# Performance work log

Measured on AMD Instinct MI355X. Metric: run time of the kernel, lower is better.

The kernel has to match this reference:

```python
import jax, jax.numpy as jnp
import numpy as np

D_HEAD = 64
KERNEL = 7


def make_neighbourhood_mask(kernel: int, ch: int, cw: int) -> jnp.ndarray:
    """Boolean mask [ch*cw, ch*cw]; True where key is inside the query's k x k window."""
    h_ramp = jnp.arange(ch)
    w_ramp = jnp.arange(cw)
    h_pos, w_pos = jnp.meshgrid(h_ramp, w_ramp, indexing='ij')  # [ch, cw]
    start_h = jnp.clip(h_pos - kernel // 2, 0, ch - kernel)[..., None, None]
    end_h = start_h + kernel
    start_w = jnp.clip(w_pos - kernel // 2, 0, cw - kernel)[..., None, None]
    end_w = start_w + kernel
    h_range = h_ramp.reshape(1, 1, ch, 1)
    w_range = w_ramp.reshape(1, 1, 1, cw)
    mask = (h_range >= start_h) & (h_range < end_h) & (w_range >= start_w) & (w_range < end_w)
    return mask.reshape(ch * cw, ch * cw)


def setup_inputs() -> dict:
    key = jax.random.key(0)
    k1, k2, k3 = jax.random.split(key, 3)
    B, H, W, D = 2, 64, 64, 384
    x = jax.random.normal(k1, (B, H, W, D), dtype=jnp.float32)
    w_qkv = jax.random.normal(k2, (3 * D, D), dtype=jnp.float32) * 0.02
    w_out = jax.random.normal(k3, (D, D), dtype=jnp.float32) * 0.02
    return {"x": x, "w_qkv": w_qkv, "w_out": w_out}


def reference(x, w_qkv, w_out):
    B, H, W, D = x.shape
    nh = D // D_HEAD
    N = H * W
    # qkv projection: Linear(D, 3D, bias=False) -> x @ w_qkv.T
    qkv = jnp.einsum('bhwd,ed->bhwe', x, w_qkv)  # [B,H,W,3D]
    # 'n h w (t nh e) -> t n nh (h w) e'
    qkv = qkv.reshape(B, N, 3, nh, D_HEAD)
    qkv = jnp.transpose(qkv, (2, 0, 3, 1, 4))  # [3, B, nh, N, e]
    q, k, v = qkv[0], qkv[1], qkv[2]
    mask = make_neighbourhood_mask(KERNEL, H, W)  # [N, N] bool
    scale = 1.0 / jnp.sqrt(jnp.asarray(D_HEAD, dtype=x.dtype))
    scores = jnp.einsum('bnqe,bnke->bnqk', q, k) * scale  # [B,nh,N,N]
    neg = jnp.asarray(jnp.finfo(scores.dtype).min, dtype=scores.dtype)
    scores = jnp.where(mask[None, None], scores, neg)
    attn = jax.nn.softmax(scores, axis=-1)
    out = jnp.einsum('bnqk,bnke->bnqe', attn, v)  # [B,nh,N,e]
    # 'n nh (h w) e -> n h w (nh e)'
    out = jnp.transpose(out, (0, 2, 1, 3)).reshape(B, H, W, D)
    return jnp.einsum('bhwd,ed->bhwe', out, w_out)
```

## Files before the change

### kernel.cpp

```cpp
#include <hip/hip_runtime.h>
#include <hip/hip_bf16.h>

typedef __attribute__((ext_vector_type(8))) short bf16x8;
typedef __attribute__((ext_vector_type(4))) short s16x4;
typedef __attribute__((ext_vector_type(4))) float fx4;

#define MFMA16(a, b, c) __builtin_amdgcn_mfma_f32_16x16x32_bf16((a), (b), (c), 0, 0, 0)

__device__ __forceinline__ short f2bf(float f) {
  unsigned u = __float_as_uint(f);
  u += 0x7fffu + ((u >> 16) & 1u);
  return (short)(u >> 16);
}

__device__ __forceinline__ bf16x8 ldu16(const short* p) {
  bf16x8 v; __builtin_memcpy(&v, p, 16); return v;
}

__device__ __forceinline__ void gl_lds16(const short* g, short* l) {
  __builtin_amdgcn_global_load_lds((const __attribute__((address_space(1))) void*)(g),
                                   (__attribute__((address_space(3))) void*)(l), 16, 0, 0);
}

__global__ __launch_bounds__(256) void convert_k(
    const float* __restrict__ x, const float* __restrict__ wq, const float* __restrict__ wo,
    short* __restrict__ xb, short* __restrict__ wb, short* __restrict__ wob) {
  const int i4 = (blockIdx.x * 256 + threadIdx.x) * 4;
  {
    float4 v = *(const float4*)(x + i4);
    s16x4 s; s[0] = f2bf(v.x); s[1] = f2bf(v.y); s[2] = f2bf(v.z); s[3] = f2bf(v.w);
    *(s16x4*)(xb + i4) = s;
  }
  if (i4 < 1152 * 384) {
    float4 v = *(const float4*)(wq + i4);
    s16x4 s; s[0] = f2bf(v.x); s[1] = f2bf(v.y); s[2] = f2bf(v.z); s[3] = f2bf(v.w);
    *(s16x4*)(wb + i4) = s;
  }
  if (i4 < 384 * 384) {
    float4 v = *(const float4*)(wo + i4);
    s16x4 s; s[0] = f2bf(v.x); s[1] = f2bf(v.y); s[2] = f2bf(v.z); s[3] = f2bf(v.w);
    *(s16x4*)(wob + i4) = s;
  }
}

__global__ __launch_bounds__(256) void qkv_gemm(
    const short* __restrict__ A, const short* __restrict__ Bw,
    short* __restrict__ qb, short* __restrict__ kb, short* __restrict__ vb) {
  __shared__ __align__(16) short As[128 * 64];
  __shared__ __align__(16) short Bs[128 * 64];
  const int orig = (blockIdx.x & 7) * 72 + (blockIdx.x >> 3);
  const int mt = orig / 9, nt = orig % 9;
  const int m0 = mt * 128, n0 = nt * 128;
  const int tid = threadIdx.x;
  const int lane = tid & 63, w = tid >> 6;
  const int wr = w >> 1, wc = w & 1;
  const int l15 = lane & 15, l4 = lane >> 4;
  const int srow = lane >> 3;
  const int scol = ((lane & 7) ^ (srow & 7)) * 8;
  const fx4 vzero = {0.f, 0.f, 0.f, 0.f};
  fx4 acc[4][4];
#pragma unroll
  for (int i = 0; i < 4; i++)
#pragma unroll
    for (int j = 0; j < 4; j++) acc[i][j] = vzero;

  for (int kt = 0; kt < 384; kt += 64) {
    __syncthreads();
#pragma unroll
    for (int q = 0; q < 4; q++) {
      gl_lds16(A  + (size_t)(m0 + w * 32 + q * 8 + srow) * 384 + kt + scol, As + (w * 32 + q * 8) * 64);
      gl_lds16(Bw + (size_t)(n0 + w * 32 + q * 8 + srow) * 384 + kt + scol, Bs + (w * 32 + q * 8) * 64);
    }
    __syncthreads();
    bf16x8 af[4][2], bfr[4][2];
#pragma unroll
    for (int i = 0; i < 4; i++) {
      const int ra = wr * 64 + i * 16 + l15;
      const int rb = wc * 64 + i * 16 + l15;
#pragma unroll
      for (int kk = 0; kk < 2; kk++) {
        af[i][kk]  = *(const bf16x8*)(As + ra * 64 + (((kk * 4 + l4) ^ (ra & 7)) * 8));
        bfr[i][kk] = *(const bf16x8*)(Bs + rb * 64 + (((kk * 4 + l4) ^ (rb & 7)) * 8));
      }
    }
#pragma unroll
    for (int i = 0; i < 4; i++)
#pragma unroll
      for (int j = 0; j < 4; j++) {
        acc[i][j] = MFMA16(af[i][0], bfr[j][0], acc[i][j]);
        acc[i][j] = MFMA16(af[i][1], bfr[j][1], acc[i][j]);
      }
  }
#pragma unroll
  for (int j = 0; j < 4; j++) {
    const int e = n0 + wc * 64 + j * 16 + l15;
    const int t = e / 384;
    const int rem = e - t * 384;
    const int head = rem >> 6, d = rem & 63;
#pragma unroll
    for (int i = 0; i < 4; i++) {
      const int mb = m0 + wr * 64 + i * 16 + l4 * 4;
      const int b = mb >> 12, pix = mb & 4095;
      if (t == 2) {
        s16x4 s4;
#pragma unroll
        for (int r = 0; r < 4; r++) s4[r] = f2bf(acc[i][j][r]);
        *(s16x4*)(vb + ((size_t)(b * 6 + head) * 64 + d) * 4096 + pix) = s4;
      } else {
        short* __restrict__ dst = (t == 0) ? qb : kb;
#pragma unroll
        for (int r = 0; r < 4; r++)
          dst[((size_t)(b * 6 + head) * 4096 + pix + r) * 64 + d] = f2bf(acc[i][j][r]);
      }
    }
  }
}

__global__ __launch_bounds__(256) void natt_k(
    const short* __restrict__ qg, const short* __restrict__ kg, const short* __restrict__ vtg,
    short* __restrict__ ob) {
  __shared__ __align__(16) short lds[224 * 72];
  short* Ks = lds;
  short* Ps = lds;

  const int bid = (blockIdx.x & 7) * 96 + (blockIdx.x >> 3);
  const int tile = bid & 63, bh = bid >> 6;
  const int h0 = (tile >> 3) * 8, w0 = (tile & 7) * 8;
  const int ph0 = max(h0 - 3, 0);
  const int pw0 = min(max(w0 - 3, 0) & ~1, 48);
  const int prows = min(h0 + 4, 57) + 7 - ph0;
  const int pcols = min(w0 + 4, 57) + 7 - pw0;
  const short* kb  = kg  + (size_t)bh * 262144;
  const short* vtb = vtg + (size_t)bh * 262144;
  const short* qb  = qg  + (size_t)bh * 262144;
  const int tid = threadIdx.x;
  const int lane = tid & 63, w = tid >> 6;
  const int l15 = lane & 15, l4 = lane >> 4;

  const int nlo = min(max(h0 + 2 * w - 3, 0), 57) - ph0;

  for (int i = tid; i < 224 * 8; i += 256) {
    const int kk = i >> 3, dc = i & 7;
    const int kr = kk >> 4, kc = kk & 15;
    const int krc = min(kr, prows - 1), kcc = min(kc, pcols - 1);
    const int pix = (ph0 + krc) * 64 + (pw0 + kcc);
    *(bf16x8*)(Ks + kk * 72 + dc * 8) = *(const bf16x8*)(kb + pix * 64 + dc * 8);
  }
  __syncthreads();

  const int qa = w * 16 + l15;
  const int qpix = (h0 + (qa >> 3)) * 64 + (w0 + (qa & 7));
  const bf16x8 aq0 = *(const bf16x8*)(qb + qpix * 64 + l4 * 8);
  const bf16x8 aq1 = *(const bf16x8*)(qb + qpix * 64 + 32 + l4 * 8);

  const fx4 vzero = {0.f, 0.f, 0.f, 0.f};
  fx4 s[8];
#pragma unroll
  for (int nj = 0; nj < 8; nj++) s[nj] = vzero;
#pragma unroll
  for (int nj = 0; nj < 8; nj++) {
    const int n = nlo + nj;
    const bf16x8 b0 = *(const bf16x8*)(Ks + (n * 16 + l15) * 72 + l4 * 8);
    const bf16x8 b1 = *(const bf16x8*)(Ks + (n * 16 + l15) * 72 + 32 + l4 * 8);
    s[nj] = MFMA16(aq0, b0, s[nj]);
    s[nj] = MFMA16(aq1, b1, s[nj]);
  }

#pragma unroll
  for (int r = 0; r < 4; r++) {
    const int q = w * 16 + l4 * 4 + r;
    const int qh = h0 + (q >> 3), qw = w0 + (q & 7);
    const int sh = min(max(qh - 3, 0), 57) - ph0;
    const int sw = min(max(qw - 3, 0), 57) - pw0;
    float m = -1e30f;
#pragma unroll
    for (int nj = 0; nj < 8; nj++) {
      const int n = nlo + nj;
      const bool valid = (n >= sh) && (n < sh + 7) && (l15 >= sw) && (l15 < sw + 7);
      const float val = valid ? s[nj][r] * 0.125f : -1e30f;
      s[nj][r] = val;
      m = fmaxf(m, val);
    }
    m = fmaxf(m, __shfl_xor(m, 1));
    m = fmaxf(m, __shfl_xor(m, 2));
    m = fmaxf(m, __shfl_xor(m, 4));
    m = fmaxf(m, __shfl_xor(m, 8));
    float sum = 0.f;
#pragma unroll
    for (int nj = 0; nj < 8; nj++) {
      const float e = __expf(s[nj][r] - m);
      s[nj][r] = e;
      sum += e;
    }
    sum += __shfl_xor(sum, 1);
    sum += __shfl_xor(sum, 2);
    sum += __shfl_xor(sum, 4);
    sum += __shfl_xor(sum, 8);
    const float inv = 1.f / sum;
#pragma unroll
    for (int nj = 0; nj < 8; nj++) s[nj][r] *= inv;
  }

  __syncthreads();

#pragma unroll
  for (int nj = 0; nj < 8; nj++)
#pragma unroll
    for (int r = 0; r < 4; r++)
      Ps[(w * 16 + l4 * 4 + r) * 136 + nj * 16 + l15] = f2bf(s[nj][r]);

  __builtin_amdgcn_wave_barrier();

  fx4 o[4];
#pragma unroll
  for (int j = 0; j < 4; j++) o[j] = vzero;
#pragma unroll
  for (int ks = 0; ks < 4; ks++) {
    const bf16x8 pa = *(const bf16x8*)(Ps + (w * 16 + l15) * 136 + ks * 32 + l4 * 8);
    const int n = nlo + 2 * ks + (l4 >> 1);
    const int vp = (ph0 + min(n, prows - 1)) * 64 + pw0 + (l4 & 1) * 8;
#pragma unroll
    for (int j = 0; j < 4; j++) {
      const bf16x8 vf = ldu16(vtb + (size_t)(j * 16 + l15) * 4096 + vp);
      o[j] = MFMA16(pa, vf, o[j]);
    }
  }

  const int b = bh / 6, head = bh % 6;
#pragma unroll
  for (int j = 0; j < 4; j++) {
    const int d = j * 16 + l15;
#pragma unroll
    for (int r = 0; r < 4; r++) {
      const int q = w * 16 + l4 * 4 + r;
      const int pix = (h0 + (q >> 3)) * 64 + (w0 + (q & 7));
      ob[(size_t)(b * 4096 + pix) * 384 + head * 64 + d] = f2bf(o[j][r]);
    }
  }
}

__global__ __launch_bounds__(256) void out_gemm(
    const short* __restrict__ A, const short* __restrict__ Bw, float* __restrict__ out) {
  __shared__ __align__(16) short As[64 * 64];
  __shared__ __align__(16) short Bs[64 * 64];
  const int orig = (blockIdx.x & 7) * 96 + (blockIdx.x >> 3);
  const int mt = orig / 6, nt = orig % 6;
  const int m0 = mt * 64, n0 = nt * 64;
  const int tid = threadIdx.x;
  const int lane = tid & 63, w = tid >> 6;
  const int wr = w >> 1, wc = w & 1;
  const int l15 = lane & 15, l4 = lane >> 4;
  const int srow = lane >> 3;
  const int scol = ((lane & 7) ^ (srow & 7)) * 8;
  const fx4 vzero = {0.f, 0.f, 0.f, 0.f};
  fx4 acc[2][2];
#pragma unroll
  for (int i = 0; i < 2; i++)
#pragma unroll
    for (int j = 0; j < 2; j++) acc[i][j] = vzero;

  for (int kt = 0; kt < 384; kt += 64) {
    __syncthreads();
#pragma unroll
    for (int q = 0; q < 2; q++) {
      gl_lds16(A  + (size_t)(m0 + w * 16 + q * 8 + srow) * 384 + kt + scol, As + (w * 16 + q * 8) * 64);
      gl_lds16(Bw + (size_t)(n0 + w * 16 + q * 8 + srow) * 384 + kt + scol, Bs + (w * 16 + q * 8) * 64);
    }
    __syncthreads();
    bf16x8 af[2][2], bfr[2][2];
#pragma unroll
    for (int i = 0; i < 2; i++) {
      const int ra = wr * 32 + i * 16 + l15;
#pragma unroll
      for (int kk = 0; kk < 2; kk++)
        af[i][kk] = *(const bf16x8*)(As + ra * 64 + (((kk * 4 + l4) ^ (ra & 7)) * 8));
    }
#pragma unroll
    for (int j = 0; j < 2; j++) {
      const int rb = wc * 32 + j * 16 + l15;
#pragma unroll
      for (int kk = 0; kk < 2; kk++)
        bfr[j][kk] = *(const bf16x8*)(Bs + rb * 64 + (((kk * 4 + l4) ^ (rb & 7)) * 8));
    }
#pragma unroll
    for (int i = 0; i < 2; i++)
#pragma unroll
      for (int j = 0; j < 2; j++) {
        acc[i][j] = MFMA16(af[i][0], bfr[j][0], acc[i][j]);
        acc[i][j] = MFMA16(af[i][1], bfr[j][1], acc[i][j]);
      }
  }
#pragma unroll
  for (int j = 0; j < 2; j++) {
    const int e = n0 + wc * 32 + j * 16 + l15;
#pragma unroll
    for (int i = 0; i < 2; i++) {
      const int mb = m0 + wr * 32 + i * 16 + l4 * 4;
#pragma unroll
      for (int r = 0; r < 4; r++)
        out[(size_t)(mb + r) * 384 + e] = acc[i][j][r];
    }
  }
}

extern "C" void kernel_launch(void* const* d_in, const int* in_sizes, int n_in,
                              void* d_out, int out_size, void* d_ws, size_t ws_size,
                              hipStream_t stream) {
  const float* x  = (const float*)d_in[0];
  const float* wq = (const float*)d_in[1];
  const float* wo = (const float*)d_in[2];
  float* out = (float*)d_out;

  short* xb  = (short*)d_ws;
  short* wb  = xb + 8192 * 384;
  short* wob = wb + 1152 * 384;
  short* qb  = wob + 384 * 384;
  short* kb  = qb + 3145728;
  short* vb  = kb + 3145728;
  short* ob  = vb + 3145728;

  convert_k<<<3072, 256, 0, stream>>>(x, wq, wo, xb, wb, wob);
  qkv_gemm<<<576, 256, 0, stream>>>(xb, wb, qb, kb, vb);
  natt_k<<<768, 256, 0, stream>>>(qb, kb, vb, ob);
  out_gemm<<<768, 256, 0, stream>>>(ob, wob, out);
}
```

Measured before the change: 45.88 us.

## Fuse fp32-to-bf16 conversion of x into QKV GEMM tile loads

Result: slower. 64.27 us (+40.1%).

```diff
diff --git a/kernel.cpp b/kernel.cpp
--- a/kernel.cpp
+++ b/kernel.cpp
@@ -13,6 +13,13 @@
   return (short)(u >> 16);
 }
 
+__device__ __forceinline__ bf16x8 cvt8f(fx4 a, fx4 b) {
+  bf16x8 r;
+  r[0] = f2bf(a[0]); r[1] = f2bf(a[1]); r[2] = f2bf(a[2]); r[3] = f2bf(a[3]);
+  r[4] = f2bf(b[0]); r[5] = f2bf(b[1]); r[6] = f2bf(b[2]); r[7] = f2bf(b[3]);
+  return r;
+}
+
 __device__ __forceinline__ bf16x8 ldu16(const short* p) {
   bf16x8 v; __builtin_memcpy(&v, p, 16); return v;
 }
@@ -21,17 +28,16 @@
   __builtin_amdgcn_global_load_lds((const __attribute__((address_space(1))) void*)(g),
                                    (__attribute__((address_space(3))) void*)(l), 16, 0, 0);
 }
+__device__ __forceinline__ void gl_lds16f(const float* g, float* l) {
+  __builtin_amdgcn_global_load_lds((const __attribute__((address_space(1))) void*)(g),
+                                   (__attribute__((address_space(3))) void*)(l), 16, 0, 0);
+}
 
 __global__ __launch_bounds__(256) void convert_k(
-    const float* __restrict__ x, const float* __restrict__ wq, const float* __restrict__ wo,
-    short* __restrict__ xb, short* __restrict__ wb, short* __restrict__ wob) {
+    const float* __restrict__ wq, const float* __restrict__ wo,
+    short* __restrict__ wb, short* __restrict__ wob) {
   const int i4 = (blockIdx.x * 256 + threadIdx.x) * 4;
   {
-    float4 v = *(const float4*)(x + i4);
-    s16x4 s; s[0] = f2bf(v.x); s[1] = f2bf(v.y); s[2] = f2bf(v.z); s[3] = f2bf(v.w);
-    *(s16x4*)(xb + i4) = s;
-  }
-  if (i4 < 1152 * 384) {
     float4 v = *(const float4*)(wq + i4);
     s16x4 s; s[0] = f2bf(v.x); s[1] = f2bf(v.y); s[2] = f2bf(v.z); s[3] = f2bf(v.w);
     *(s16x4*)(wb + i4) = s;
@@ -44,9 +50,9 @@
 }
 
 __global__ __launch_bounds__(256) void qkv_gemm(
-    const short* __restrict__ A, const short* __restrict__ Bw,
+    const float* __restrict__ Ax, const short* __restrict__ Bw,
     short* __restrict__ qb, short* __restrict__ kb, short* __restrict__ vb) {
-  __shared__ __align__(16) short As[128 * 64];
+  __shared__ __align__(16) float Af[128 * 64];
   __shared__ __align__(16) short Bs[128 * 64];
   const int orig = (blockIdx.x & 7) * 72 + (blockIdx.x >> 3);
   const int mt = orig / 9, nt = orig % 9;
@@ -55,6 +61,8 @@
   const int lane = tid & 63, w = tid >> 6;
   const int wr = w >> 1, wc = w & 1;
   const int l15 = lane & 15, l4 = lane >> 4;
+  const int ar = lane >> 4;
+  const int ac = lane & 15;
   const int srow = lane >> 3;
   const int scol = ((lane & 7) ^ (srow & 7)) * 8;
   const fx4 vzero = {0.f, 0.f, 0.f, 0.f};
@@ -67,19 +75,27 @@
   for (int kt = 0; kt < 384; kt += 64) {
     __syncthreads();
 #pragma unroll
-    for (int q = 0; q < 4; q++) {
-      gl_lds16(A  + (size_t)(m0 + w * 32 + q * 8 + srow) * 384 + kt + scol, As + (w * 32 + q * 8) * 64);
+    for (int q = 0; q < 8; q++) {
+      const int rr = q * 4 + ar;
+      const int sc = (ac ^ (rr & 15)) * 4;
+      gl_lds16f(Ax + (size_t)(m0 + w * 32 + rr) * 384 + kt + sc, Af + (w * 32 + q * 4) * 64);
+    }
+#pragma unroll
+    for (int q = 0; q < 4; q++)
       gl_lds16(Bw + (size_t)(n0 + w * 32 + q * 8 + srow) * 384 + kt + scol, Bs + (w * 32 + q * 8) * 64);
-    }
     __syncthreads();
     bf16x8 af[4][2], bfr[4][2];
 #pragma unroll
     for (int i = 0; i < 4; i++) {
       const int ra = wr * 64 + i * 16 + l15;
       const int rb = wc * 64 + i * 16 + l15;
+      const int swa = ra & 15;
 #pragma unroll
       for (int kk = 0; kk < 2; kk++) {
-        af[i][kk]  = *(const bf16x8*)(As + ra * 64 + (((kk * 4 + l4) ^ (ra & 7)) * 8));
+        const int c0 = kk * 8 + l4 * 2;
+        const fx4 f0 = *(const fx4*)(Af + ra * 64 + ((c0 ^ swa) * 4));
+        const fx4 f1 = *(const fx4*)(Af + ra * 64 + (((c0 + 1) ^ swa) * 4));
+        af[i][kk] = cvt8f(f0, f1);
         bfr[i][kk] = *(const bf16x8*)(Bs + rb * 64 + (((kk * 4 + l4) ^ (rb & 7)) * 8));
       }
     }
@@ -139,6 +155,11 @@
 
   const int nlo = min(max(h0 + 2 * w - 3, 0), 57) - ph0;
 
+  const int qa = w * 16 + l15;
+  const int qpix = (h0 + (qa >> 3)) * 64 + (w0 + (qa & 7));
+  const bf16x8 aq0 = *(const bf16x8*)(qb + qpix * 64 + l4 * 8);
+  const bf16x8 aq1 = *(const bf16x8*)(qb + qpix * 64 + 32 + l4 * 8);
+
   for (int i = tid; i < 224 * 8; i += 256) {
     const int kk = i >> 3, dc = i & 7;
     const int kr = kk >> 4, kc = kk & 15;
@@ -147,11 +168,6 @@
     *(bf16x8*)(Ks + kk * 72 + dc * 8) = *(const bf16x8*)(kb + pix * 64 + dc * 8);
   }
   __syncthreads();
-
-  const int qa = w * 16 + l15;
-  const int qpix = (h0 + (qa >> 3)) * 64 + (w0 + (qa & 7));
-  const bf16x8 aq0 = *(const bf16x8*)(qb + qpix * 64 + l4 * 8);
-  const bf16x8 aq1 = *(const bf16x8*)(qb + qpix * 64 + 32 + l4 * 8);
 
   const fx4 vzero = {0.f, 0.f, 0.f, 0.f};
   fx4 s[8];
@@ -311,16 +327,15 @@
   const float* wo = (const float*)d_in[2];
   float* out = (float*)d_out;
 
-  short* xb  = (short*)d_ws;
-  short* wb  = xb + 8192 * 384;
+  short* wb  = (short*)d_ws;
   short* wob = wb + 1152 * 384;
   short* qb  = wob + 384 * 384;
   short* kb  = qb + 3145728;
   short* vb  = kb + 3145728;
   short* ob  = vb + 3145728;
 
-  convert_k<<<3072, 256, 0, stream>>>(x, wq, wo, xb, wb, wob);
-  qkv_gemm<<<576, 256, 0, stream>>>(xb, wb, qb, kb, vb);
+  convert_k<<<432, 256, 0, stream>>>(wq, wo, wb, wob);
+  qkv_gemm<<<576, 256, 0, stream>>>(x, wb, qb, kb, vb);
   natt_k<<<768, 256, 0, stream>>>(qb, kb, vb, ob);
   out_gemm<<<768, 256, 0, stream>>>(ob, wob, out);
 }
```
